# Kernel tuning notes

Hardware: AMD Instinct MI355X
Metric: run time of the kernel (lower is better)

The kernel has to match this reference:

```python
import jax, jax.numpy as jnp
import numpy as np
import math

B, A, I, O = 4096, 32, 256, 256


def setup_inputs() -> dict:
    key = jax.random.key(0)
    kx, kw, kb = jax.random.split(key, 3)
    x = jax.random.normal(kx, (B, A, I), dtype=jnp.float32)
    # kaiming_uniform_(a=sqrt(5)) on [A, O, I]: fan_in = I, bound = sqrt(6/((1+5)*I)) = 1/sqrt(I)
    wb = 1.0 / math.sqrt(I)
    weight = jax.random.uniform(kw, (A, O, I), minval=-wb, maxval=wb, dtype=jnp.float32)
    bb = 1.0 / math.sqrt(I)
    bias = jax.random.uniform(kb, (A, O), minval=-bb, maxval=bb, dtype=jnp.float32)
    return {"x": x, "weight": weight, "bias": bias}


def reference(x, weight, bias):
    # per-assignment batched GEMM: weight [A,O,I], x [B,A,I] -> [B,A,O]
    return jnp.einsum('aoi,bai->bao', weight, x) + bias
```

## Files before the change

### kernel.cpp

```cpp
#include <hip/hip_runtime.h>

typedef __attribute__((ext_vector_type(4))) float f32x4;
typedef __attribute__((ext_vector_type(8))) short bf16x8;

constexpr int Bsz = 4096, Asz = 32, Isz = 256, Osz = 256;
constexpr int NT = 32;

__device__ inline unsigned cvtpk(float lo, float hi) {
    unsigned r;
    asm("v_cvt_pk_bf16_f32 %0, %1, %2" : "=v"(r) : "v"(lo), "v"(hi));
    return r;
}

__device__ inline void gl_lds16(const void* g, void* l) {
    __builtin_amdgcn_global_load_lds((const __attribute__((address_space(1))) void*)g,
                                     (__attribute__((address_space(3))) void*)l, 16, 0, 0);
}

__global__ __launch_bounds__(512, 2) void al_gemm(const float* __restrict__ x,
                                                  const float* __restrict__ wsrc,
                                                  const float* __restrict__ bias,
                                                  float* __restrict__ out)
{
    __shared__ char sA[2][16384];
    __shared__ char sB[131072];

    const int p  = blockIdx.x;
    const int a  = (p & 7) * 4 + ((p >> 3) & 3);
    const int b0 = (p >> 5) * 512;

    const int t    = threadIdx.x;
    const int w    = t >> 6;
    const int lane = t & 63;
    const int llo  = lane & 15, lhi = lane >> 4;

    const int r0 = 2 * w, r1 = 2 * w + 1;
    const float* asrc0 = x + ((size_t)(b0 + r0) * Asz + a) * Isz
                           + ((lane & 56) | ((lane & 7) ^ (r0 & 7))) * 4;
    const float* asrc1 = x + ((size_t)(b0 + r1) * Asz + a) * Isz
                           + ((lane & 56) | ((lane & 7) ^ (r1 & 7))) * 4;

#define ISSUE(tn) {                                                            \
    const size_t o_ = (size_t)(tn) * (16 * Asz * Isz);                         \
    char* d_ = &sA[(tn) & 1][0];                                               \
    gl_lds16(asrc0 + o_, d_ + r0 * 1024);                                      \
    gl_lds16(asrc1 + o_, d_ + r1 * 1024); }

    ISSUE(0);
    __builtin_amdgcn_sched_barrier(0);

    {
        const float* wa = wsrc + (size_t)a * (Osz * Isz);
#pragma unroll
        for (int i = 0; i < 16; ++i) {
            const int s     = i * 512 + t;
            const int o     = s >> 5;
            const int kt    = (s >> 2) & 7;
            const int nf    = s >> 9;
            const int lane_ = (o & 15) | ((s & 3) << 4);
            f32x4 lo = *(const f32x4*)(wa + (size_t)s * 8);
            f32x4 hi = *(const f32x4*)(wa + (size_t)s * 8 + 4);
            union { bf16x8 v; unsigned u[4]; } r;
            r.u[0] = cvtpk(lo[0], lo[1]); r.u[1] = cvtpk(lo[2], lo[3]);
            r.u[2] = cvtpk(hi[0], hi[1]); r.u[3] = cvtpk(hi[2], hi[3]);
            *(bf16x8*)&sB[(((kt * 16 + nf) * 64) + lane_) * 16] = r.v;
        }
    }

    const float bv0 = bias[a * Osz + w * 32 + llo];
    const float bv1 = bias[a * Osz + w * 32 + 16 + llo];

    __syncthreads();

    const int abase = llo * 1024 + (((2 * lhi) ^ (llo & 7)) << 4);

    for (int tn = 0; tn < NT; ++tn) {
        if (tn < NT - 1) ISSUE(tn + 1);
        __builtin_amdgcn_sched_barrier(0);

        const char* As = &sA[tn & 1][0];
        f32x4 acc0 = (f32x4)(bv0), acc1 = (f32x4)(bv1);
        __builtin_amdgcn_s_setprio(1);
#pragma unroll
        for (int kt = 0; kt < 8; ++kt) {
            const int ad = abase + kt * 128;
            f32x4 lo = *(const f32x4*)(As + ad);
            f32x4 hi = *(const f32x4*)(As + (ad ^ 16));
            union { bf16x8 v; unsigned u[4]; } r;
            r.u[0] = cvtpk(lo[0], lo[1]); r.u[1] = cvtpk(lo[2], lo[3]);
            r.u[2] = cvtpk(hi[0], hi[1]); r.u[3] = cvtpk(hi[2], hi[3]);
            const bf16x8 aF = r.v;
            const bf16x8 bF0 = *(const bf16x8*)&sB[(kt * 16 + 2 * w) * 1024 + lane * 16];
            const bf16x8 bF1 = *(const bf16x8*)&sB[(kt * 16 + 2 * w + 1) * 1024 + lane * 16];
            acc0 = __builtin_amdgcn_mfma_f32_16x16x32_bf16(aF, bF0, acc0, 0, 0, 0);
            acc1 = __builtin_amdgcn_mfma_f32_16x16x32_bf16(aF, bF1, acc1, 0, 0, 0);
        }
        __builtin_amdgcn_s_setprio(0);

        const int trow = b0 + tn * 16 + lhi * 4;
        float* op = out + ((size_t)trow * Asz + a) * Osz + w * 32 + llo;
#pragma unroll
        for (int r2 = 0; r2 < 4; ++r2) {
            op[(size_t)r2 * Asz * Osz]      = acc0[r2];
            op[(size_t)r2 * Asz * Osz + 16] = acc1[r2];
        }

        if (tn < NT - 1) {
            __builtin_amdgcn_sched_barrier(0);
            asm volatile("s_waitcnt vmcnt(8)" ::: "memory");
            __builtin_amdgcn_sched_barrier(0);
            __builtin_amdgcn_s_barrier();
        }
    }
#undef ISSUE
}

extern "C" void kernel_launch(void* const* d_in, const int* in_sizes, int n_in,
                              void* d_out, int out_size, void* d_ws, size_t ws_size,
                              hipStream_t stream) {
    const float* x    = (const float*)d_in[0];
    const float* w    = (const float*)d_in[1];
    const float* bias = (const float*)d_in[2];
    float* out        = (float*)d_out;
    al_gemm<<<dim3(256), dim3(512), 0, stream>>>(x, w, bias, out);
}
```

Before: 64.69 us.

## Convert activation tiles to bf16 once via register staging instead of direct LDS loads

Activation tiles are no longer loaded straight into LDS as fp32 with global_load_lds. Each thread now loads them into registers, converts to bf16 once and writes a swizzled bf16 tile into a half-size LDS buffer. This removes the repeated per-wave fp32-to-bf16 conversions and halves the LDS reads in the MFMA loop. The cost is a register round trip, a full __syncthreads per tile, and the global load latency now being exposed through VGPRs rather than async LDS transfers.

```diff
diff --git a/kernel.cpp b/kernel.cpp
--- a/kernel.cpp
+++ b/kernel.cpp
@@ -1,6 +1,7 @@
 #include <hip/hip_runtime.h>
 
 typedef __attribute__((ext_vector_type(4))) float f32x4;
+typedef __attribute__((ext_vector_type(2))) unsigned u32x2;
 typedef __attribute__((ext_vector_type(8))) short bf16x8;
 
 constexpr int Bsz = 4096, Asz = 32, Isz = 256, Osz = 256;
@@ -12,17 +13,12 @@
     return r;
 }
 
-__device__ inline void gl_lds16(const void* g, void* l) {
-    __builtin_amdgcn_global_load_lds((const __attribute__((address_space(1))) void*)g,
-                                     (__attribute__((address_space(3))) void*)l, 16, 0, 0);
-}
-
 __global__ __launch_bounds__(512, 2) void al_gemm(const float* __restrict__ x,
                                                   const float* __restrict__ wsrc,
                                                   const float* __restrict__ bias,
                                                   float* __restrict__ out)
 {
-    __shared__ char sA[2][16384];
+    __shared__ char sA[2][8192];
     __shared__ char sB[131072];
 
     const int p  = blockIdx.x;
@@ -34,20 +30,16 @@
     const int lane = t & 63;
     const int llo  = lane & 15, lhi = lane >> 4;
 
-    const int r0 = 2 * w, r1 = 2 * w + 1;
-    const float* asrc0 = x + ((size_t)(b0 + r0) * Asz + a) * Isz
-                           + ((lane & 56) | ((lane & 7) ^ (r0 & 7))) * 4;
-    const float* asrc1 = x + ((size_t)(b0 + r1) * Asz + a) * Isz
-                           + ((lane & 56) | ((lane & 7) ^ (r1 & 7))) * 4;
+    const int lr0 = 2 * w, lr1 = 2 * w + 1;
+    const float* fs0 = x + ((size_t)(b0 + lr0) * Asz + a) * Isz + lane * 4;
+    const float* fs1 = x + ((size_t)(b0 + lr1) * Asz + a) * Isz + lane * 4;
+    const int wa0 = lr0 * 512 + (((lane >> 1) ^ lr0) << 4) + (lane & 1) * 8;
+    const int wa1 = lr1 * 512 + (((lane >> 1) ^ lr1) << 4) + (lane & 1) * 8;
 
-#define ISSUE(tn) {                                                            \
-    const size_t o_ = (size_t)(tn) * (16 * Asz * Isz);                         \
-    char* d_ = &sA[(tn) & 1][0];                                               \
-    gl_lds16(asrc0 + o_, d_ + r0 * 1024);                                      \
-    gl_lds16(asrc1 + o_, d_ + r1 * 1024); }
-
-    ISSUE(0);
-    __builtin_amdgcn_sched_barrier(0);
+    f32x4 L0, L1;
+    L0 = *(const f32x4*)fs0;
+    L1 = *(const f32x4*)fs1;
+    asm volatile("" : "+v"(L0), "+v"(L1));
 
     {
         const float* wa = wsrc + (size_t)a * (Osz * Isz);
@@ -70,26 +62,25 @@
     const float bv0 = bias[a * Osz + w * 32 + llo];
     const float bv1 = bias[a * Osz + w * 32 + 16 + llo];
 
+    *(u32x2*)&sA[0][wa0] = (u32x2){cvtpk(L0[0], L0[1]), cvtpk(L0[2], L0[3])};
+    *(u32x2*)&sA[0][wa1] = (u32x2){cvtpk(L1[0], L1[1]), cvtpk(L1[2], L1[3])};
+
     __syncthreads();
 
-    const int abase = llo * 1024 + (((2 * lhi) ^ (llo & 7)) << 4);
-
     for (int tn = 0; tn < NT; ++tn) {
-        if (tn < NT - 1) ISSUE(tn + 1);
-        __builtin_amdgcn_sched_barrier(0);
+        if (tn < NT - 1) {
+            const size_t o_ = (size_t)(tn + 1) * (16 * Asz * Isz);
+            L0 = *(const f32x4*)(fs0 + o_);
+            L1 = *(const f32x4*)(fs1 + o_);
+            asm volatile("" : "+v"(L0), "+v"(L1));
+        }
 
         const char* As = &sA[tn & 1][0];
         f32x4 acc0 = (f32x4)(bv0), acc1 = (f32x4)(bv1);
         __builtin_amdgcn_s_setprio(1);
 #pragma unroll
         for (int kt = 0; kt < 8; ++kt) {
-            const int ad = abase + kt * 128;
-            f32x4 lo = *(const f32x4*)(As + ad);
-            f32x4 hi = *(const f32x4*)(As + (ad ^ 16));
-            union { bf16x8 v; unsigned u[4]; } r;
-            r.u[0] = cvtpk(lo[0], lo[1]); r.u[1] = cvtpk(lo[2], lo[3]);
-            r.u[2] = cvtpk(hi[0], hi[1]); r.u[3] = cvtpk(hi[2], hi[3]);
-            const bf16x8 aF = r.v;
+            const bf16x8 aF = *(const bf16x8*)&As[llo * 512 + ((((kt * 4) + lhi) ^ llo) << 4)];
             const bf16x8 bF0 = *(const bf16x8*)&sB[(kt * 16 + 2 * w) * 1024 + lane * 16];
             const bf16x8 bF1 = *(const bf16x8*)&sB[(kt * 16 + 2 * w + 1) * 1024 + lane * 16];
             acc0 = __builtin_amdgcn_mfma_f32_16x16x32_bf16(aF, bF0, acc0, 0, 0, 0);
@@ -106,13 +97,13 @@
         }
 
         if (tn < NT - 1) {
-            __builtin_amdgcn_sched_barrier(0);
-            asm volatile("s_waitcnt vmcnt(8)" ::: "memory");
-            __builtin_amdgcn_sched_barrier(0);
-            __builtin_amdgcn_s_barrier();
+            char* Ad = &sA[(tn + 1) & 1][0];
+            *(u32x2*)&Ad[wa0] = (u32x2){cvtpk(L0[0], L0[1]), cvtpk(L0[2], L0[3])};
+            *(u32x2*)&Ad[wa1] = (u32x2){cvtpk(L1[0], L1[1]), cvtpk(L1[2], L1[3])};
         }
+
+        __syncthreads();
     }
-#undef ISSUE
 }
 
 extern "C" void kernel_launch(void* const* d_in, const int* in_sizes, int n_in,
```

Measured after the change: 60.18 us. 7.0% less time.
